# Kernel tuning notes

Hardware: AMD Instinct MI355X
Metric: run time of the kernel (lower is better)

Reference implementation:

```python
import jax, jax.numpy as jnp
import numpy as np

B, IN_DIM, D, C = 16384, 1024, 256, 100


def setup_inputs() -> dict:
    key = jax.random.key(0)
    k1, k2, k3, k4 = jax.random.split(key, 4)
    x = jax.random.normal(k1, (B, IN_DIM), dtype=jnp.float32)
    W = jax.random.normal(k2, (IN_DIM, D), dtype=jnp.float32) * (1.0 / np.sqrt(IN_DIM))
    b = jax.random.normal(k3, (D,), dtype=jnp.float32) * 0.01
    P = jax.random.normal(k4, (C, D), dtype=jnp.float32)  # class prototypes [C, D]
    return {"x": x, "W": W, "b": b, "P": P}


def reference(x, W, b, P):
    # Encoder: Z = x @ W + b  -> [B, D]
    Z = x @ W + b
    d = Z.shape[-1]
    # MSE(r, p) = mean((r - p)^2) = (|r|^2 - 2 r.p + |p|^2) / D
    # Computed via expansion to avoid the [B, C, D] broadcast intermediate.
    sq = (
        jnp.sum(Z * Z, axis=-1, keepdims=True)      # [B, 1]
        - 2.0 * (Z @ P.T)                            # [B, C]
        + jnp.sum(P * P, axis=-1)[None, :]           # [1, C]
    )
    return -sq / d  # [B, C]
```

## Files before the change

### kernel.cpp

```cpp
#include <hip/hip_runtime.h>

#define BATCH 16384
#define KDIM  1024
#define DDIM  256
#define CNUM  100
#define CPAD  112

typedef __bf16 bf16x4 __attribute__((ext_vector_type(4)));
typedef __bf16 bf16x8 __attribute__((ext_vector_type(8)));
typedef float  floatx4 __attribute__((ext_vector_type(4)));

static __device__ __forceinline__ unsigned short f2b(float f) {
    return __builtin_bit_cast(unsigned short, (__bf16)f);
}

static __device__ __forceinline__ void gload_lds16(const unsigned short* g,
                                                   unsigned short* l) {
    __builtin_amdgcn_global_load_lds(
        (const __attribute__((address_space(1))) unsigned int*)g,
        (__attribute__((address_space(3))) unsigned int*)l, 16, 0, 0);
}

__global__ __launch_bounds__(256) void prep(const float* __restrict__ W,
                                            const float* __restrict__ P,
                                            unsigned short* __restrict__ Wt,
                                            unsigned short* __restrict__ Pbf,
                                            float* __restrict__ pnorm2) {
    __shared__ float T[32][33];
    const int bid = blockIdx.x;
    if (bid < 256) {
        const int k0 = (bid & 31) * 32;
        const int n0 = (bid >> 5) * 32;
        const int j  = threadIdx.x & 31;
        const int i0 = threadIdx.x >> 5;
#pragma unroll
        for (int l = 0; l < 4; ++l) {
            int i = i0 + l * 8;
            T[i][j] = W[(k0 + i) * DDIM + n0 + j];
        }
        __syncthreads();
#pragma unroll
        for (int l = 0; l < 4; ++l) {
            int i = i0 + l * 8;
            Wt[(n0 + i) * KDIM + k0 + j] = f2b(T[j][i]);
        }
    } else {
        const int wave = threadIdx.x >> 6;
        const int lane = threadIdx.x & 63;
        const int c = (bid - 256) * 4 + wave;
        float s = 0.f;
#pragma unroll
        for (int jj = 0; jj < 4; ++jj) {
            int d = jj * 64 + lane;
            float v = (c < CNUM) ? P[c * DDIM + d] : 0.f;
            Pbf[c * DDIM + d] = f2b(v);
            s += v * v;
        }
#pragma unroll
        for (int m = 1; m < 64; m <<= 1) s += __shfl_xor(s, m, 64);
        if (lane == 0) pnorm2[c] = s;
    }
}

__global__ __launch_bounds__(256, 4) void fused_main(
    const float* __restrict__ x, const float* __restrict__ bias,
    const unsigned short* __restrict__ Wt, const unsigned short* __restrict__ Pbf,
    const float* __restrict__ pnorm2, float* __restrict__ out)
{
    __shared__ unsigned short U[18432];
    unsigned short* As = U;
    unsigned short* Bs = U + 2048;
    unsigned short* Zs = U;
    __shared__ float rn2[4][32];

    const int tid  = threadIdx.x;
    const int wave = tid >> 6;
    const int lane = tid & 63;
    const int lm   = lane & 15;
    const int lq   = lane >> 4;
    const int r0   = blockIdx.x * 32;

    const int rowA = tid >> 3;
    const int kbA  = tid & 7;
    const float* gA = x + (r0 + rowA) * KDIM + kbA * 8;
    const int ldsA = rowA * 64 + ((kbA ^ (rowA & 7)) * 8);

    const int gkb = (lane & 7) ^ ((lane >> 3) & 7);
    const unsigned short* gB = Wt + (wave * 64 + (lane >> 3)) * KDIM + gkb * 8;
    unsigned short* ldsB = Bs + (wave * 64) * 64;

    const int sw0 = ((0 * 4 + lq) ^ (lm & 7)) * 8;
    const int sw1 = ((1 * 4 + lq) ^ (lm & 7)) * 8;

    floatx4 acc[2][4];
#pragma unroll
    for (int g = 0; g < 2; ++g)
#pragma unroll
        for (int f = 0; f < 4; ++f) { acc[g][f][0]=0.f; acc[g][f][1]=0.f; acc[g][f][2]=0.f; acc[g][f][3]=0.f; }

    floatx4 pa0 = *(const floatx4*)(gA);
    floatx4 pa1 = *(const floatx4*)(gA + 4);

#pragma unroll 2
    for (int kk = 0; kk < KDIM; kk += 64) {
        __syncthreads();
#pragma unroll
        for (int j = 0; j < 8; ++j)
            gload_lds16(gB + j * 8 * KDIM + kk, ldsB + j * 8 * 64);
        bf16x8 ha;
        ha[0] = (__bf16)pa0[0]; ha[1] = (__bf16)pa0[1];
        ha[2] = (__bf16)pa0[2]; ha[3] = (__bf16)pa0[3];
        ha[4] = (__bf16)pa1[0]; ha[5] = (__bf16)pa1[1];
        ha[6] = (__bf16)pa1[2]; ha[7] = (__bf16)pa1[3];
        *(bf16x8*)&As[ldsA] = ha;
        __syncthreads();
        if (kk + 64 < KDIM) {
            pa0 = *(const floatx4*)(gA + kk + 64);
            pa1 = *(const floatx4*)(gA + kk + 68);
        }
#pragma unroll
        for (int kf = 0; kf < 2; ++kf) {
            const int sw = kf ? sw1 : sw0;
            bf16x8 a0 = *(const bf16x8*)&As[lm * 64 + sw];
            bf16x8 a1 = *(const bf16x8*)&As[(16 + lm) * 64 + sw];
#pragma unroll
            for (int f = 0; f < 4; ++f) {
                bf16x8 bfr = *(const bf16x8*)&Bs[(wave * 64 + f * 16 + lm) * 64 + sw];
                acc[0][f] = __builtin_amdgcn_mfma_f32_16x16x32_bf16(a0, bfr, acc[0][f], 0, 0, 0);
                acc[1][f] = __builtin_amdgcn_mfma_f32_16x16x32_bf16(a1, bfr, acc[1][f], 0, 0, 0);
            }
        }
    }

#pragma unroll
    for (int f = 0; f < 4; ++f) {
        float bb = bias[wave * 64 + f * 16 + lm];
#pragma unroll
        for (int g = 0; g < 2; ++g)
#pragma unroll
            for (int r = 0; r < 4; ++r) acc[g][f][r] += bb;
    }

#pragma unroll
    for (int g = 0; g < 2; ++g) {
        float s0 = 0.f, s1 = 0.f, s2 = 0.f, s3 = 0.f;
#pragma unroll
        for (int f = 0; f < 4; ++f) {
            s0 += acc[g][f][0] * acc[g][f][0];
            s1 += acc[g][f][1] * acc[g][f][1];
            s2 += acc[g][f][2] * acc[g][f][2];
            s3 += acc[g][f][3] * acc[g][f][3];
        }
#pragma unroll
        for (int m = 1; m < 16; m <<= 1) {
            s0 += __shfl_xor(s0, m, 64);
            s1 += __shfl_xor(s1, m, 64);
            s2 += __shfl_xor(s2, m, 64);
            s3 += __shfl_xor(s3, m, 64);
        }
        if (lm == 0) {
            int rl = g * 16 + lq * 4;
            rn2[wave][rl + 0] = s0;
            rn2[wave][rl + 1] = s1;
            rn2[wave][rl + 2] = s2;
            rn2[wave][rl + 3] = s3;
        }
    }

    __syncthreads();

#pragma unroll
    for (int g = 0; g < 2; ++g)
#pragma unroll
        for (int f = 0; f < 4; ++f) {
            int col = wave * 64 + f * 16 + lm;
#pragma unroll
            for (int r = 0; r < 4; ++r)
                Zs[(g * 16 + lq * 4 + r) * 264 + col] = f2b(acc[g][f][r]);
        }
    __syncthreads();

#pragma unroll
    for (int t = 0; t < 2; ++t) {
        const int ct = wave * 2 + t;
        if (ct < 7) {
            floatx4 acc2[2];
#pragma unroll
            for (int nf = 0; nf < 2; ++nf) { acc2[nf][0]=0.f; acc2[nf][1]=0.f; acc2[nf][2]=0.f; acc2[nf][3]=0.f; }
            const unsigned short* gP = Pbf + (ct * 16 + lm) * DDIM + lq * 8;
#pragma unroll
            for (int ks = 0; ks < 8; ++ks) {
                bf16x8 ap = *(const bf16x8*)(gP + ks * 32);
#pragma unroll
                for (int nf = 0; nf < 2; ++nf) {
                    bf16x8 bz = *(const bf16x8*)&Zs[(nf * 16 + lm) * 264 + ks * 32 + lq * 8];
                    acc2[nf] = __builtin_amdgcn_mfma_f32_16x16x32_bf16(ap, bz, acc2[nf], 0, 0, 0);
                }
            }
            int c0 = ct * 16 + lq * 4;
            if (c0 < CNUM) {
                floatx4 pn = *(const floatx4*)(pnorm2 + c0);
#pragma unroll
                for (int nf = 0; nf < 2; ++nf) {
                    int rl = nf * 16 + lm;
                    float rn = rn2[0][rl] + rn2[1][rl] + rn2[2][rl] + rn2[3][rl];
                    floatx4 o;
#pragma unroll
                    for (int r = 0; r < 4; ++r)
                        o[r] = (2.f * acc2[nf][r] - rn - pn[r]) * (1.f / 256.f);
                    *(floatx4*)&out[(r0 + rl) * CNUM + c0] = o;
                }
            }
        }
    }
}

extern "C" void kernel_launch(void* const* d_in, const int* in_sizes, int n_in,
                              void* d_out, int out_size, void* d_ws, size_t ws_size,
                              hipStream_t stream) {
    const float* x = (const float*)d_in[0];
    const float* W = (const float*)d_in[1];
    const float* b = (const float*)d_in[2];
    const float* P = (const float*)d_in[3];
    float* out = (float*)d_out;

    unsigned short* Wt  = (unsigned short*)d_ws;
    unsigned short* Pbf = Wt + KDIM * DDIM;
    float* pn2 = (float*)(Pbf + CPAD * DDIM);

    prep<<<256 + CPAD / 4, 256, 0, stream>>>(W, P, Wt, Pbf, pn2);
    fused_main<<<BATCH / 32, 256, 0, stream>>>(x, b, Wt, Pbf, pn2, out);
}
```

Before: 124.1 us.

## Double-buffer LDS tiles in encoder GEMM to overlap loads with MFMA

The A and B LDS tiles of the x@W GEMM become double-buffered. The next K-slice's global-to-LDS loads and bf16 conversion are issued before the current slice's MFMAs, so only one barrier per iteration is needed instead of two. Shared memory per block roughly doubles, so the occupancy hint drops from 4 to 2 blocks per CU, trading fewer resident waves for overlap of transfers with compute. The separate barrier before the epilogue is removed, relying on the loop-end barrier to protect the overlapping Zs region.

```diff
diff --git a/kernel.cpp b/kernel.cpp
--- a/kernel.cpp
+++ b/kernel.cpp
@@ -62,14 +62,12 @@
     }
 }
 
-__global__ __launch_bounds__(256, 4) void fused_main(
+__global__ __launch_bounds__(256, 2) void fused_main(
     const float* __restrict__ x, const float* __restrict__ bias,
     const unsigned short* __restrict__ Wt, const unsigned short* __restrict__ Pbf,
     const float* __restrict__ pnorm2, float* __restrict__ out)
 {
-    __shared__ unsigned short U[18432];
-    unsigned short* As = U;
-    unsigned short* Bs = U + 2048;
+    __shared__ unsigned short U[36864];
     unsigned short* Zs = U;
     __shared__ float rn2[4][32];
 
@@ -87,7 +85,6 @@
 
     const int gkb = (lane & 7) ^ ((lane >> 3) & 7);
     const unsigned short* gB = Wt + (wave * 64 + (lane >> 3)) * KDIM + gkb * 8;
-    unsigned short* ldsB = Bs + (wave * 64) * 64;
 
     const int sw0 = ((0 * 4 + lq) ^ (lm & 7)) * 8;
     const int sw1 = ((1 * 4 + lq) ^ (lm & 7)) * 8;
@@ -98,38 +95,58 @@
 #pragma unroll
         for (int f = 0; f < 4; ++f) { acc[g][f][0]=0.f; acc[g][f][1]=0.f; acc[g][f][2]=0.f; acc[g][f][3]=0.f; }
 
-    floatx4 pa0 = *(const floatx4*)(gA);
-    floatx4 pa1 = *(const floatx4*)(gA + 4);
+    {
+        floatx4 q0 = *(const floatx4*)(gA);
+        floatx4 q1 = *(const floatx4*)(gA + 4);
+#pragma unroll
+        for (int j = 0; j < 8; ++j)
+            gload_lds16(gB + j * 8 * KDIM, U + 4096 + (wave * 64 + j * 8) * 64);
+        bf16x8 ha;
+        ha[0] = (__bf16)q0[0]; ha[1] = (__bf16)q0[1];
+        ha[2] = (__bf16)q0[2]; ha[3] = (__bf16)q0[3];
+        ha[4] = (__bf16)q1[0]; ha[5] = (__bf16)q1[1];
+        ha[6] = (__bf16)q1[2]; ha[7] = (__bf16)q1[3];
+        *(bf16x8*)&U[ldsA] = ha;
+    }
+    floatx4 pa0 = *(const floatx4*)(gA + 64);
+    floatx4 pa1 = *(const floatx4*)(gA + 68);
+    __syncthreads();
 
 #pragma unroll 2
     for (int kk = 0; kk < KDIM; kk += 64) {
-        __syncthreads();
-#pragma unroll
-        for (int j = 0; j < 8; ++j)
-            gload_lds16(gB + j * 8 * KDIM + kk, ldsB + j * 8 * 64);
-        bf16x8 ha;
-        ha[0] = (__bf16)pa0[0]; ha[1] = (__bf16)pa0[1];
-        ha[2] = (__bf16)pa0[2]; ha[3] = (__bf16)pa0[3];
-        ha[4] = (__bf16)pa1[0]; ha[5] = (__bf16)pa1[1];
-        ha[6] = (__bf16)pa1[2]; ha[7] = (__bf16)pa1[3];
-        *(bf16x8*)&As[ldsA] = ha;
-        __syncthreads();
+        const int cur = (kk >> 6) & 1;
+        const int nxt = cur ^ 1;
+        unsigned short* As_c = U + cur * 2048;
+        unsigned short* Bs_c = U + 4096 + cur * 16384;
         if (kk + 64 < KDIM) {
-            pa0 = *(const floatx4*)(gA + kk + 64);
-            pa1 = *(const floatx4*)(gA + kk + 68);
+            unsigned short* Bs_n = U + 4096 + nxt * 16384;
+#pragma unroll
+            for (int j = 0; j < 8; ++j)
+                gload_lds16(gB + j * 8 * KDIM + kk + 64, Bs_n + (wave * 64 + j * 8) * 64);
+            bf16x8 ha;
+            ha[0] = (__bf16)pa0[0]; ha[1] = (__bf16)pa0[1];
+            ha[2] = (__bf16)pa0[2]; ha[3] = (__bf16)pa0[3];
+            ha[4] = (__bf16)pa1[0]; ha[5] = (__bf16)pa1[1];
+            ha[6] = (__bf16)pa1[2]; ha[7] = (__bf16)pa1[3];
+            *(bf16x8*)&(U + nxt * 2048)[ldsA] = ha;
+            if (kk + 128 < KDIM) {
+                pa0 = *(const floatx4*)(gA + kk + 128);
+                pa1 = *(const floatx4*)(gA + kk + 132);
+            }
         }
 #pragma unroll
         for (int kf = 0; kf < 2; ++kf) {
             const int sw = kf ? sw1 : sw0;
-            bf16x8 a0 = *(const bf16x8*)&As[lm * 64 + sw];
-            bf16x8 a1 = *(const bf16x8*)&As[(16 + lm) * 64 + sw];
+            bf16x8 a0 = *(const bf16x8*)&As_c[lm * 64 + sw];
+            bf16x8 a1 = *(const bf16x8*)&As_c[(16 + lm) * 64 + sw];
 #pragma unroll
             for (int f = 0; f < 4; ++f) {
-                bf16x8 bfr = *(const bf16x8*)&Bs[(wave * 64 + f * 16 + lm) * 64 + sw];
+                bf16x8 bfr = *(const bf16x8*)&Bs_c[(wave * 64 + f * 16 + lm) * 64 + sw];
                 acc[0][f] = __builtin_amdgcn_mfma_f32_16x16x32_bf16(a0, bfr, acc[0][f], 0, 0, 0);
                 acc[1][f] = __builtin_amdgcn_mfma_f32_16x16x32_bf16(a1, bfr, acc[1][f], 0, 0, 0);
             }
         }
+        __syncthreads();
     }
 
 #pragma unroll
@@ -166,8 +183,6 @@
             rn2[wave][rl + 3] = s3;
         }
     }
-
-    __syncthreads();
 
 #pragma unroll
     for (int g = 0; g < 2; ++g)
```

New measurement: 116.3 us. -6.3%, faster.
